# Performance work log

Measured on AMD Instinct MI355X. Metric: run time of the kernel, lower is better.

Reference implementation:

```python
import jax, jax.numpy as jnp
import numpy as np

B, T, E, H, OUT, L = 128, 512, 256, 512, 9, 2


def setup_inputs() -> dict:
    key = jax.random.key(0)
    ks = jax.random.split(key, 6)
    def lin(k, shape, fan_in):
        return (jax.random.normal(k, shape, jnp.float32) / np.float32(np.sqrt(fan_in)))
    return {
        "embeddings": jax.random.normal(ks[0], (B, T, E), jnp.float32),
        "W_w": lin(ks[1], (H, E), E),
        "W_b": jnp.zeros((H,), jnp.float32),
        "Uk_w": lin(ks[2], (L, H, H), H),
        "Uk_b": jnp.zeros((L, H), jnp.float32),
        "Wk_w": lin(ks[3], (L - 1, H, H), H),
        "Wk_b": jnp.zeros((L - 1, H), jnp.float32),
        "V_w": lin(ks[4], (OUT, H), H),
        "V_b": jnp.zeros((OUT,), jnp.float32),
    }


def reference(embeddings, W_w, W_b, Uk_w, Uk_b, Wk_w, Wk_b, V_w, V_b):
    n_layers = Uk_w.shape[0]
    bsz = embeddings.shape[0]
    hid = W_w.shape[0]
    # Input projection W(x_t) is time-independent: do it once as a big GEMM. [B,T,H]
    xproj = jnp.einsum('bte,he->bth', embeddings, W_w) + W_b

    def step(z_prev, xp_t):
        # z_prev: [L, B, H]; xp_t: [B, H]
        z = jnp.tanh(xp_t + z_prev[0] @ Uk_w[0].T + Uk_b[0])
        zs = [z]
        for l in range(n_layers - 1):
            # NOTE: original code uses Uks[l] (not Uks[l+1]) here -- reproduced faithfully.
            z = jnp.tanh(z @ Wk_w[l].T + Wk_b[l] + z_prev[l + 1] @ Uk_w[l].T + Uk_b[l])
            zs.append(z)
        y = z @ V_w.T + V_b  # [B, OUT]
        return jnp.stack(zs, 0), y

    z0 = jnp.zeros((n_layers, bsz, hid), embeddings.dtype)
    _, ys = jax.lax.scan(step, z0, jnp.swapaxes(xproj, 0, 1))  # ys: [T, B, OUT]
    return jnp.swapaxes(ys, 0, 1)  # [B, T, OUT]
```

## Files before the change

### kernel.cpp

```cpp
#include <hip/hip_runtime.h>
#include <hip/hip_fp16.h>

typedef _Float16 half8 __attribute__((ext_vector_type(8)));
typedef float floatx4 __attribute__((ext_vector_type(4)));


union H8 { half8 v; unsigned long long u[2]; };

__device__ __forceinline__ unsigned long long agload(const unsigned long long* p) {
  return __hip_atomic_load(p, __ATOMIC_RELAXED, __HIP_MEMORY_SCOPE_AGENT);
}
__device__ __forceinline__ void agstore(unsigned long long* p, unsigned long long v) {
  __hip_atomic_store(p, v, __ATOMIC_RELAXED, __HIP_MEMORY_SCOPE_AGENT);
}
__device__ __forceinline__ bool valid16(unsigned long long u) {
  return (unsigned)((unsigned)(u & 0xFFFFull) - 0x3C00u) <= 0x600u;
}

__global__ void prep_small(const float* __restrict__ Vw, const float* __restrict__ Vb,
                           const float* __restrict__ Wb, const float* __restrict__ Ukb,
                           const float* __restrict__ Wkb, const float* __restrict__ Ukw,
                           const float* __restrict__ Wkw, _Float16* __restrict__ V16,
                           float* __restrict__ bxp, float* __restrict__ bc,
                           float* __restrict__ sums) {
  int i = blockIdx.x * blockDim.x + threadIdx.x;
  if (i < 16 * 512) {
    int o = i >> 9, k = i & 511;
    V16[i] = (_Float16)(o < 9 ? Vw[o * 512 + k] : 0.0f);
  }
  if (i < 512) {
    bxp[i] = Wb[i] + Ukb[i];
    bc[i]  = Wkb[i] + Ukb[i];
  }
  if (i < 1024) {
    const float* row = (i < 512) ? Ukw + (size_t)i * 512 : Wkw + (size_t)(i - 512) * 512;
    float s = 0.f;
    for (int k = 0; k < 512; k += 4) {
      float4 v = *(const float4*)(row + k);
      s += (float)(_Float16)v.x + (float)(_Float16)v.y + (float)(_Float16)v.z + (float)(_Float16)v.w;
    }
    sums[i] = s;
  } else if (i < 1040) {
    int o = i - 1024;
    float s = 0.f;
    if (o < 9) {
      const float* row = Vw + (size_t)o * 512;
      for (int k = 0; k < 512; k += 4) {
        float4 v = *(const float4*)(row + k);
        s += (float)(_Float16)v.x + (float)(_Float16)v.y + (float)(_Float16)v.z + (float)(_Float16)v.w;
      }
    }
    sums[i] = (o < 9 ? Vb[o] : 0.f) - 2.f * s;
  }
}

__global__ __launch_bounds__(256) void gemm_xp(const float* __restrict__ Aptr,
                                               const float* __restrict__ Bptr,
                                               _Float16* __restrict__ Cout,
                                               const float* __restrict__ bias) {
  const int K = 256;
  __shared__ __align__(16) _Float16 As[128][40];
  __shared__ __align__(16) _Float16 Bs[128][40];
  const int tid = threadIdx.x;
  const int bm = blockIdx.x, bn = blockIdx.y;
  const int w = tid >> 6, lane = tid & 63;
  const int m = lane & 15, q = lane >> 4;

  floatx4 acc[2][8];
#pragma unroll
  for (int i = 0; i < 2; ++i)
#pragma unroll
    for (int j = 0; j < 8; ++j) acc[i][j] = (floatx4){0.f, 0.f, 0.f, 0.f};

  for (int kt = 0; kt < (K >> 5); ++kt) {
    const int k0 = kt << 5;
    __syncthreads();
#pragma unroll
    for (int it = 0; it < 2; ++it) {
      int idx = tid + it * 256;
      int row = idx >> 2, ch = idx & 3;
      size_t gA = (size_t)(bm * 128 + row) * K + (k0 + ch * 8);
      const float4* p = (const float4*)(Aptr + gA);
      float4 f0 = p[0], f1 = p[1];
      *(half8*)&As[row][ch * 8] =
          (half8){(_Float16)f0.x, (_Float16)f0.y, (_Float16)f0.z, (_Float16)f0.w,
                  (_Float16)f1.x, (_Float16)f1.y, (_Float16)f1.z, (_Float16)f1.w};
      size_t gB = (size_t)(bn * 128 + row) * K + (k0 + ch * 8);
      const float4* pb = (const float4*)(Bptr + gB);
      float4 g0 = pb[0], g1 = pb[1];
      *(half8*)&Bs[row][ch * 8] =
          (half8){(_Float16)g0.x, (_Float16)g0.y, (_Float16)g0.z, (_Float16)g0.w,
                  (_Float16)g1.x, (_Float16)g1.y, (_Float16)g1.z, (_Float16)g1.w};
    }
    __syncthreads();
    half8 a[2], b[8];
#pragma unroll
    for (int i = 0; i < 2; ++i) a[i] = *(const half8*)&As[w * 32 + i * 16 + m][q * 8];
#pragma unroll
    for (int j = 0; j < 8; ++j) b[j] = *(const half8*)&Bs[j * 16 + m][q * 8];
#pragma unroll
    for (int i = 0; i < 2; ++i)
#pragma unroll
      for (int j = 0; j < 8; ++j)
        acc[i][j] = __builtin_amdgcn_mfma_f32_16x16x32_f16(a[i], b[j], acc[i][j], 0, 0, 0);
  }
#pragma unroll
  for (int i = 0; i < 2; ++i)
#pragma unroll
    for (int j = 0; j < 8; ++j) {
      int col = bn * 128 + j * 16 + m;
      float bv = bias[col];
#pragma unroll
      for (int rr = 0; rr < 4; ++rr) {
        int row = bm * 128 + w * 32 + i * 16 + q * 4 + rr;
        size_t orow = (size_t)(row & 511) * 128 + (row >> 9);
        Cout[orow * 512 + col] = (_Float16)(acc[i][j][rr] + bv);
      }
    }
}

template <int SLEEP>
__device__ __forceinline__ void stage_tile(const _Float16* srcTile, _Float16* dst, int tid) {
  const unsigned long long* src = (const unsigned long long*)srcTile;
  unsigned long long g[8];
#pragma unroll
  for (int j = 0; j < 4; ++j) {
    g[2 * j] = agload(src + 2 * (tid + j * 256));
    g[2 * j + 1] = agload(src + 2 * (tid + j * 256) + 1);
  }
  unsigned need = 0;
#pragma unroll
  for (int i = 0; i < 8; ++i)
    if (!valid16(g[i])) need |= (1u << i);
  while (need) {
    if (SLEEP) __builtin_amdgcn_s_sleep(1);
#pragma unroll
    for (int i = 0; i < 8; ++i)
      if (need & (1u << i)) {
        unsigned long long v = agload(src + 2 * (tid + (i >> 1) * 256) + (i & 1));
        if (valid16(v)) { g[i] = v; need &= ~(1u << i); }
      }
  }
#pragma unroll
  for (int j = 0; j < 4; ++j) {
    H8 t;
    t.u[0] = g[2 * j];
    t.u[1] = g[2 * j + 1];
    *(half8*)&dst[(tid + j * 256) * 8] = t.v;
  }
}

__global__ __launch_bounds__(256, 1) void rnn_fused2(const float* __restrict__ Uw,
                                                     const float* __restrict__ Wkw,
                                                     const _Float16* __restrict__ xp,
                                                     _Float16* __restrict__ z0f,
                                                     _Float16* __restrict__ z1f,
                                                     const float* __restrict__ bc,
                                                     const float* __restrict__ sums) {
  __shared__ __align__(16) _Float16 az[8192];
  __shared__ __align__(16) _Float16 azs[8192];
  __shared__ __align__(16) _Float16 zo[16][136];
  const int tid = threadIdx.x;
  const int layer = blockIdx.x >> 5, bt = blockIdx.x & 7, ct = (blockIdx.x >> 3) & 3;
  const int lane = tid & 63, w = tid >> 6, m = lane & 15, q = lane >> 4;
  const int colbase = ct * 128 + w * 32;

  half8 ufr[2][16], wfr[2][16];
#pragma unroll
  for (int t = 0; t < 2; ++t) {
    const float* up = Uw + (size_t)(colbase + t * 16 + m) * 512 + q * 8;
    const float* wp = Wkw + (size_t)(colbase + t * 16 + m) * 512 + q * 8;
#pragma unroll
    for (int kk = 0; kk < 16; ++kk) {
      float4 f0 = *(const float4*)(up + kk * 32), f1 = *(const float4*)(up + kk * 32 + 4);
      ufr[t][kk] = (half8){(_Float16)f0.x, (_Float16)f0.y, (_Float16)f0.z, (_Float16)f0.w,
                           (_Float16)f1.x, (_Float16)f1.y, (_Float16)f1.z, (_Float16)f1.w};
      if (layer) {
        float4 g0 = *(const float4*)(wp + kk * 32), g1 = *(const float4*)(wp + kk * 32 + 4);
        wfr[t][kk] = (half8){(_Float16)g0.x, (_Float16)g0.y, (_Float16)g0.z, (_Float16)g0.w,
                             (_Float16)g1.x, (_Float16)g1.y, (_Float16)g1.z, (_Float16)g1.w};
      }
    }
  }
  const float corrU[2] = {-2.f * sums[colbase + m], -2.f * sums[colbase + 16 + m]};
  float cw[2] = {0.f, 0.f};
  if (layer) {
    cw[0] = -2.f * sums[512 + colbase + m] + bc[colbase + m];
    cw[1] = -2.f * sums[512 + colbase + 16 + m] + bc[colbase + 16 + m];
  }

  const int c16l = tid >> 4, b15 = tid & 15;
  _Float16* zout = layer ? z1f : z0f;

  if (layer) stage_tile<1>(z0f + (size_t)bt * 8192, azs, tid);

  for (int s = 0; s < 512; ++s) {
    float pin[8];
    if (layer == 0) {
      const _Float16* xb = xp + (size_t)s * 65536 + (size_t)(bt * 16) * 512;
#pragma unroll
      for (int t = 0; t < 2; ++t)
#pragma unroll
        for (int rr = 0; rr < 4; ++rr)
          pin[t * 4 + rr] = (float)xb[(size_t)(q * 4 + rr) * 512 + colbase + t * 16 + m];
    }

    floatx4 wk[2];
    wk[0] = (floatx4){0.f, 0.f, 0.f, 0.f};
    wk[1] = (floatx4){0.f, 0.f, 0.f, 0.f};
    if (layer) {
      __syncthreads();
      unsigned long long g[8];
      unsigned need = 0;
      const unsigned long long* src =
          (const unsigned long long*)(z1f + ((size_t)(s - 1) * 8 + bt) * 8192);
      if (s > 0) {
#pragma unroll
        for (int j = 0; j < 4; ++j) {
          g[2 * j] = agload(src + 2 * (tid + j * 256));
          g[2 * j + 1] = agload(src + 2 * (tid + j * 256) + 1);
        }
      }
#pragma unroll
      for (int kk = 0; kk < 16; ++kk) {
        half8 a = *(const half8*)&azs[((kk * 4 + q) * 16 + m) * 8];
        wk[0] = __builtin_amdgcn_mfma_f32_16x16x32_f16(a, wfr[0][kk], wk[0], 0, 0, 0);
        wk[1] = __builtin_amdgcn_mfma_f32_16x16x32_f16(a, wfr[1][kk], wk[1], 0, 0, 0);
      }
      if (s > 0) {
#pragma unroll
        for (int i = 0; i < 8; ++i)
          if (!valid16(g[i])) need |= (1u << i);
        while (need) {
#pragma unroll
          for (int i = 0; i < 8; ++i)
            if (need & (1u << i)) {
              unsigned long long v = agload(src + 2 * (tid + (i >> 1) * 256) + (i & 1));
              if (valid16(v)) { g[i] = v; need &= ~(1u << i); }
            }
        }
#pragma unroll
        for (int j = 0; j < 4; ++j) {
          H8 t;
          t.u[0] = g[2 * j];
          t.u[1] = g[2 * j + 1];
          *(half8*)&az[(tid + j * 256) * 8] = t.v;
        }
      }
    } else {
      if (s > 0) stage_tile<0>(z0f + ((size_t)(s - 1) * 8 + bt) * 8192, az, tid);
    }
    __syncthreads();

    floatx4 acc[2][2];
    acc[0][0] = (floatx4){0.f, 0.f, 0.f, 0.f};
    acc[0][1] = (floatx4){0.f, 0.f, 0.f, 0.f};
    acc[1][0] = (floatx4){0.f, 0.f, 0.f, 0.f};
    acc[1][1] = (floatx4){0.f, 0.f, 0.f, 0.f};
    if (s > 0) {
#pragma unroll
      for (int kk = 0; kk < 16; ++kk) {
        half8 a = *(const half8*)&az[((kk * 4 + q) * 16 + m) * 8];
        acc[0][kk & 1] = __builtin_amdgcn_mfma_f32_16x16x32_f16(a, ufr[0][kk], acc[0][kk & 1], 0, 0, 0);
        acc[1][kk & 1] = __builtin_amdgcn_mfma_f32_16x16x32_f16(a, ufr[1][kk], acc[1][kk & 1], 0, 0, 0);
      }
    }
#pragma unroll
    for (int t = 0; t < 2; ++t)
#pragma unroll
      for (int rr = 0; rr < 4; ++rr) {
        float x = layer ? (wk[t][rr] + cw[t]) : pin[t * 4 + rr];
        if (s > 0) x += acc[t][0][rr] + acc[t][1][rr] + corrU[t];
        float e = __builtin_exp2f(x * 2.885390081777927f);
        float enc = 3.f - 2.f * __builtin_amdgcn_rcpf(e + 1.f);
        zo[q * 4 + rr][w * 32 + t * 16 + m] = (_Float16)enc;
      }
    __syncthreads();
    {
      H8 pv;
      pv.v = *(const half8*)&zo[b15][c16l * 8];
      unsigned long long* dst =
          (unsigned long long*)((char*)zout +
                                (((size_t)s * 8 + bt) * 1024 + (size_t)(ct * 16 + c16l) * 16 + b15) * 16);
      agstore(dst, pv.u[0]);
      agstore(dst + 1, pv.u[1]);
    }
    if (layer && s < 511)
      stage_tile<1>(z0f + ((size_t)(s + 1) * 8 + bt) * 8192, azs, tid);
  }
}

__global__ __launch_bounds__(64) void out_gemm(const _Float16* __restrict__ z1,
                                               const _Float16* __restrict__ V16,
                                               const float* __restrict__ bco,
                                               float* __restrict__ out) {
  __shared__ __align__(16) _Float16 zt[16][520];
  __shared__ __align__(16) _Float16 vt[16][520];
  const int tid = threadIdx.x;
  const int m = tid & 15, q = tid >> 4;
  const size_t r0 = (size_t)blockIdx.x * 16;
  for (int idx = tid; idx < 1024; idx += 64) {
    int row = idx >> 6, ch = idx & 63;
    int r = (int)(r0 + row), t = r >> 7, b = r & 127;
    size_t off = (size_t)(t * 8 + (b >> 4)) * 8192 + (size_t)ch * 128 + (b & 15) * 8;
    *(half8*)&zt[row][ch * 8] = *(const half8*)&z1[off];
    *(half8*)&vt[row][ch * 8] = *(const half8*)&V16[(size_t)row * 512 + ch * 8];
  }
  __syncthreads();
  floatx4 acc = {0.f, 0.f, 0.f, 0.f};
#pragma unroll
  for (int kk = 0; kk < 16; ++kk) {
    half8 a = *(const half8*)&zt[m][kk * 32 + q * 8];
    half8 b = *(const half8*)&vt[m][kk * 32 + q * 8];
    acc = __builtin_amdgcn_mfma_f32_16x16x32_f16(a, b, acc, 0, 0, 0);
  }
  if (m < 9) {
#pragma unroll
    for (int rr = 0; rr < 4; ++rr) {
      size_t r = r0 + q * 4 + rr;
      size_t t = r >> 7, b = r & 127;
      out[(b * 512 + t) * 9 + m] = acc[rr] + bco[m];
    }
  }
}

extern "C" void kernel_launch(void* const* d_in, const int* in_sizes, int n_in,
                              void* d_out, int out_size, void* d_ws, size_t ws_size,
                              hipStream_t stream) {
  const float* emb = (const float*)d_in[0];
  const float* Ww  = (const float*)d_in[1];
  const float* Wb  = (const float*)d_in[2];
  const float* Ukw = (const float*)d_in[3];
  const float* Ukb = (const float*)d_in[4];
  const float* Wkw = (const float*)d_in[5];
  const float* Wkb = (const float*)d_in[6];
  const float* Vw  = (const float*)d_in[7];
  const float* Vb  = (const float*)d_in[8];
  float* out = (float*)d_out;

  char* ws = (char*)d_ws;
  _Float16* xp   = (_Float16*)(ws + 0);
  _Float16* z0f  = (_Float16*)(ws + 67108864);
  _Float16* z1f  = (_Float16*)(ws + 134217728);
  _Float16* V16  = (_Float16*)(ws + 201326592);
  float* bxp     = (float*)(ws + 201342976);
  float* bc      = (float*)(ws + 201345024);
  float* sums    = (float*)(ws + 201347072);

  hipLaunchKernelGGL(prep_small, dim3(32), dim3(256), 0, stream,
                     Vw, Vb, Wb, Ukb, Wkb, Ukw, Wkw, V16, bxp, bc, sums);
  hipLaunchKernelGGL(gemm_xp, dim3(512, 4), dim3(256), 0, stream, emb, Ww, xp, bxp);
  hipLaunchKernelGGL(rnn_fused2, dim3(64), dim3(256), 0, stream,
                     Ukw, Wkw, xp, z0f, z1f, bc, sums);
  hipLaunchKernelGGL(out_gemm, dim3(4096), dim3(64), 0, stream, z1f, V16, sums + 1024, out);
}
```

Before: 1.753 ms.

## Fuse input projection into recurrent kernel and load state directly into registers

Drops the separate input-projection GEMM. Layer-0 blocks now hold W_w fragments in registers and compute the embedding projection with MFMA at each step, so the fp16 xp buffer is never written or read back. The state exchange also changes: each wave reads the previous state straight from global memory into MFMA operand registers using per-element polling, and prefetches the next step's tiles right after storing its own. This removes the shared-memory staging and block-wide __syncthreads. The cost is higher register pressure, extra per-step embedding loads on the serial critical path, and more polling traffic.

```diff
diff --git a/kernel.cpp b/kernel.cpp
--- a/kernel.cpp
+++ b/kernel.cpp
@@ -54,239 +54,202 @@
   }
 }
 
-__global__ __launch_bounds__(256) void gemm_xp(const float* __restrict__ Aptr,
-                                               const float* __restrict__ Bptr,
-                                               _Float16* __restrict__ Cout,
-                                               const float* __restrict__ bias) {
-  const int K = 256;
-  __shared__ __align__(16) _Float16 As[128][40];
-  __shared__ __align__(16) _Float16 Bs[128][40];
-  const int tid = threadIdx.x;
-  const int bm = blockIdx.x, bn = blockIdx.y;
-  const int w = tid >> 6, lane = tid & 63;
-  const int m = lane & 15, q = lane >> 4;
-
-  floatx4 acc[2][8];
-#pragma unroll
-  for (int i = 0; i < 2; ++i)
-#pragma unroll
-    for (int j = 0; j < 8; ++j) acc[i][j] = (floatx4){0.f, 0.f, 0.f, 0.f};
-
-  for (int kt = 0; kt < (K >> 5); ++kt) {
-    const int k0 = kt << 5;
-    __syncthreads();
-#pragma unroll
-    for (int it = 0; it < 2; ++it) {
-      int idx = tid + it * 256;
-      int row = idx >> 2, ch = idx & 3;
-      size_t gA = (size_t)(bm * 128 + row) * K + (k0 + ch * 8);
-      const float4* p = (const float4*)(Aptr + gA);
-      float4 f0 = p[0], f1 = p[1];
-      *(half8*)&As[row][ch * 8] =
-          (half8){(_Float16)f0.x, (_Float16)f0.y, (_Float16)f0.z, (_Float16)f0.w,
-                  (_Float16)f1.x, (_Float16)f1.y, (_Float16)f1.z, (_Float16)f1.w};
-      size_t gB = (size_t)(bn * 128 + row) * K + (k0 + ch * 8);
-      const float4* pb = (const float4*)(Bptr + gB);
-      float4 g0 = pb[0], g1 = pb[1];
-      *(half8*)&Bs[row][ch * 8] =
-          (half8){(_Float16)g0.x, (_Float16)g0.y, (_Float16)g0.z, (_Float16)g0.w,
-                  (_Float16)g1.x, (_Float16)g1.y, (_Float16)g1.z, (_Float16)g1.w};
-    }
-    __syncthreads();
-    half8 a[2], b[8];
-#pragma unroll
-    for (int i = 0; i < 2; ++i) a[i] = *(const half8*)&As[w * 32 + i * 16 + m][q * 8];
-#pragma unroll
-    for (int j = 0; j < 8; ++j) b[j] = *(const half8*)&Bs[j * 16 + m][q * 8];
-#pragma unroll
-    for (int i = 0; i < 2; ++i)
-#pragma unroll
-      for (int j = 0; j < 8; ++j)
-        acc[i][j] = __builtin_amdgcn_mfma_f32_16x16x32_f16(a[i], b[j], acc[i][j], 0, 0, 0);
-  }
-#pragma unroll
-  for (int i = 0; i < 2; ++i)
-#pragma unroll
-    for (int j = 0; j < 8; ++j) {
-      int col = bn * 128 + j * 16 + m;
-      float bv = bias[col];
-#pragma unroll
-      for (int rr = 0; rr < 4; ++rr) {
-        int row = bm * 128 + w * 32 + i * 16 + q * 4 + rr;
-        size_t orow = (size_t)(row & 511) * 128 + (row >> 9);
-        Cout[orow * 512 + col] = (_Float16)(acc[i][j][rr] + bv);
-      }
-    }
-}
-
-template <int SLEEP>
-__device__ __forceinline__ void stage_tile(const _Float16* srcTile, _Float16* dst, int tid) {
-  const unsigned long long* src = (const unsigned long long*)srcTile;
-  unsigned long long g[8];
-#pragma unroll
-  for (int j = 0; j < 4; ++j) {
-    g[2 * j] = agload(src + 2 * (tid + j * 256));
-    g[2 * j + 1] = agload(src + 2 * (tid + j * 256) + 1);
-  }
-  unsigned need = 0;
-#pragma unroll
-  for (int i = 0; i < 8; ++i)
-    if (!valid16(g[i])) need |= (1u << i);
-  while (need) {
-    if (SLEEP) __builtin_amdgcn_s_sleep(1);
-#pragma unroll
-    for (int i = 0; i < 8; ++i)
-      if (need & (1u << i)) {
-        unsigned long long v = agload(src + 2 * (tid + (i >> 1) * 256) + (i & 1));
-        if (valid16(v)) { g[i] = v; need &= ~(1u << i); }
-      }
-  }
-#pragma unroll
-  for (int j = 0; j < 4; ++j) {
-    H8 t;
-    t.u[0] = g[2 * j];
-    t.u[1] = g[2 * j + 1];
-    *(half8*)&dst[(tid + j * 256) * 8] = t.v;
-  }
-}
-
-__global__ __launch_bounds__(256, 1) void rnn_fused2(const float* __restrict__ Uw,
-                                                     const float* __restrict__ Wkw,
-                                                     const _Float16* __restrict__ xp,
-                                                     _Float16* __restrict__ z0f,
-                                                     _Float16* __restrict__ z1f,
-                                                     const float* __restrict__ bc,
-                                                     const float* __restrict__ sums) {
-  __shared__ __align__(16) _Float16 az[8192];
-  __shared__ __align__(16) _Float16 azs[8192];
-  __shared__ __align__(16) _Float16 zo[16][136];
+__global__ __launch_bounds__(256, 1) void rnn_fused2(
+    const float* __restrict__ Uw, const float* __restrict__ Wkw,
+    const float* __restrict__ emb, const float* __restrict__ Ww,
+    _Float16* __restrict__ z0f, _Float16* __restrict__ z1f,
+    const float* __restrict__ bxp, const float* __restrict__ bc,
+    const float* __restrict__ sums) {
+  __shared__ __align__(16) _Float16 zo[4][16][40];
   const int tid = threadIdx.x;
   const int layer = blockIdx.x >> 5, bt = blockIdx.x & 7, ct = (blockIdx.x >> 3) & 3;
   const int lane = tid & 63, w = tid >> 6, m = lane & 15, q = lane >> 4;
   const int colbase = ct * 128 + w * 32;
-
-  half8 ufr[2][16], wfr[2][16];
+  const int cs = ct * 4 + w;
+  const int lbase = (q * 16 + m) * 2;
+
+  half8 ufr[2][16], wfr[2][16], wxr[2][8];
 #pragma unroll
   for (int t = 0; t < 2; ++t) {
     const float* up = Uw + (size_t)(colbase + t * 16 + m) * 512 + q * 8;
-    const float* wp = Wkw + (size_t)(colbase + t * 16 + m) * 512 + q * 8;
 #pragma unroll
     for (int kk = 0; kk < 16; ++kk) {
       float4 f0 = *(const float4*)(up + kk * 32), f1 = *(const float4*)(up + kk * 32 + 4);
       ufr[t][kk] = (half8){(_Float16)f0.x, (_Float16)f0.y, (_Float16)f0.z, (_Float16)f0.w,
                            (_Float16)f1.x, (_Float16)f1.y, (_Float16)f1.z, (_Float16)f1.w};
-      if (layer) {
+    }
+  }
+  if (layer == 0) {
+#pragma unroll
+    for (int t = 0; t < 2; ++t) {
+      const float* wp = Ww + (size_t)(colbase + t * 16 + m) * 256 + q * 8;
+#pragma unroll
+      for (int kk = 0; kk < 8; ++kk) {
+        float4 f0 = *(const float4*)(wp + kk * 32), f1 = *(const float4*)(wp + kk * 32 + 4);
+        wxr[t][kk] = (half8){(_Float16)f0.x, (_Float16)f0.y, (_Float16)f0.z, (_Float16)f0.w,
+                             (_Float16)f1.x, (_Float16)f1.y, (_Float16)f1.z, (_Float16)f1.w};
+      }
+    }
+  } else {
+#pragma unroll
+    for (int t = 0; t < 2; ++t) {
+      const float* wp = Wkw + (size_t)(colbase + t * 16 + m) * 512 + q * 8;
+#pragma unroll
+      for (int kk = 0; kk < 16; ++kk) {
         float4 g0 = *(const float4*)(wp + kk * 32), g1 = *(const float4*)(wp + kk * 32 + 4);
         wfr[t][kk] = (half8){(_Float16)g0.x, (_Float16)g0.y, (_Float16)g0.z, (_Float16)g0.w,
                              (_Float16)g1.x, (_Float16)g1.y, (_Float16)g1.z, (_Float16)g1.w};
       }
     }
   }
+
   const float corrU[2] = {-2.f * sums[colbase + m], -2.f * sums[colbase + 16 + m]};
-  float cw[2] = {0.f, 0.f};
+  float cw[2] = {0.f, 0.f}, bxpv[2] = {0.f, 0.f};
   if (layer) {
     cw[0] = -2.f * sums[512 + colbase + m] + bc[colbase + m];
     cw[1] = -2.f * sums[512 + colbase + 16 + m] + bc[colbase + 16 + m];
-  }
-
-  const int c16l = tid >> 4, b15 = tid & 15;
-  _Float16* zout = layer ? z1f : z0f;
-
-  if (layer) stage_tile<1>(z0f + (size_t)bt * 8192, azs, tid);
+  } else {
+    bxpv[0] = bxp[colbase + m];
+    bxpv[1] = bxp[colbase + 16 + m];
+  }
+
+  unsigned long long* const selfU = (unsigned long long*)(layer ? z1f : z0f);
+  const unsigned long long* const z0U = (const unsigned long long*)z0f;
+
+  unsigned long long ga[16][2];
+  unsigned long long gb[16][2];
+  if (layer) {
+    const unsigned long long* srcb0 = z0U + (size_t)bt * 2048;
+#pragma unroll
+    for (int i = 0; i < 16; ++i) {
+      gb[i][0] = agload(srcb0 + i * 128 + lbase);
+      gb[i][1] = agload(srcb0 + i * 128 + lbase + 1);
+    }
+  }
 
   for (int s = 0; s < 512; ++s) {
-    float pin[8];
+    float4 ef[8][2];
     if (layer == 0) {
-      const _Float16* xb = xp + (size_t)s * 65536 + (size_t)(bt * 16) * 512;
-#pragma unroll
-      for (int t = 0; t < 2; ++t)
-#pragma unroll
-        for (int rr = 0; rr < 4; ++rr)
-          pin[t * 4 + rr] = (float)xb[(size_t)(q * 4 + rr) * 512 + colbase + t * 16 + m];
-    }
-
-    floatx4 wk[2];
-    wk[0] = (floatx4){0.f, 0.f, 0.f, 0.f};
-    wk[1] = (floatx4){0.f, 0.f, 0.f, 0.f};
+      const float* ep = emb + (size_t)(bt * 16 + m) * 131072 + (size_t)s * 256 + q * 8;
+#pragma unroll
+      for (int kk = 0; kk < 8; ++kk) {
+        ef[kk][0] = *(const float4*)(ep + kk * 32);
+        ef[kk][1] = *(const float4*)(ep + kk * 32 + 4);
+      }
+    }
+
+    floatx4 wk[2][2];
+    wk[0][0] = wk[0][1] = wk[1][0] = wk[1][1] = (floatx4){0.f, 0.f, 0.f, 0.f};
     if (layer) {
-      __syncthreads();
-      unsigned long long g[8];
+      const unsigned long long* srcb = z0U + ((size_t)s * 8 + bt) * 2048;
       unsigned need = 0;
-      const unsigned long long* src =
-          (const unsigned long long*)(z1f + ((size_t)(s - 1) * 8 + bt) * 8192);
-      if (s > 0) {
-#pragma unroll
-        for (int j = 0; j < 4; ++j) {
-          g[2 * j] = agload(src + 2 * (tid + j * 256));
-          g[2 * j + 1] = agload(src + 2 * (tid + j * 256) + 1);
-        }
+#pragma unroll
+      for (int i = 0; i < 16; ++i) {
+        if (!valid16(gb[i][0])) need |= (1u << (2 * i));
+        if (!valid16(gb[i][1])) need |= (2u << (2 * i));
+      }
+      while (need) {
+#pragma unroll
+        for (int i = 0; i < 16; ++i) {
+          if (need & (1u << (2 * i))) gb[i][0] = agload(srcb + i * 128 + lbase);
+          if (need & (2u << (2 * i))) gb[i][1] = agload(srcb + i * 128 + lbase + 1);
+        }
+        unsigned nn = 0;
+#pragma unroll
+        for (int i = 0; i < 16; ++i) {
+          if ((need & (1u << (2 * i))) && !valid16(gb[i][0])) nn |= (1u << (2 * i));
+          if ((need & (2u << (2 * i))) && !valid16(gb[i][1])) nn |= (2u << (2 * i));
+        }
+        need = nn;
       }
 #pragma unroll
       for (int kk = 0; kk < 16; ++kk) {
-        half8 a = *(const half8*)&azs[((kk * 4 + q) * 16 + m) * 8];
-        wk[0] = __builtin_amdgcn_mfma_f32_16x16x32_f16(a, wfr[0][kk], wk[0], 0, 0, 0);
-        wk[1] = __builtin_amdgcn_mfma_f32_16x16x32_f16(a, wfr[1][kk], wk[1], 0, 0, 0);
-      }
-      if (s > 0) {
-#pragma unroll
-        for (int i = 0; i < 8; ++i)
-          if (!valid16(g[i])) need |= (1u << i);
-        while (need) {
-#pragma unroll
-          for (int i = 0; i < 8; ++i)
-            if (need & (1u << i)) {
-              unsigned long long v = agload(src + 2 * (tid + (i >> 1) * 256) + (i & 1));
-              if (valid16(v)) { g[i] = v; need &= ~(1u << i); }
-            }
-        }
-#pragma unroll
-        for (int j = 0; j < 4; ++j) {
-          H8 t;
-          t.u[0] = g[2 * j];
-          t.u[1] = g[2 * j + 1];
-          *(half8*)&az[(tid + j * 256) * 8] = t.v;
-        }
-      }
-    } else {
-      if (s > 0) stage_tile<0>(z0f + ((size_t)(s - 1) * 8 + bt) * 8192, az, tid);
-    }
-    __syncthreads();
+        H8 a; a.u[0] = gb[kk][0]; a.u[1] = gb[kk][1];
+        wk[0][kk & 1] = __builtin_amdgcn_mfma_f32_16x16x32_f16(a.v, wfr[0][kk], wk[0][kk & 1], 0, 0, 0);
+        wk[1][kk & 1] = __builtin_amdgcn_mfma_f32_16x16x32_f16(a.v, wfr[1][kk], wk[1][kk & 1], 0, 0, 0);
+      }
+    }
 
     floatx4 acc[2][2];
-    acc[0][0] = (floatx4){0.f, 0.f, 0.f, 0.f};
-    acc[0][1] = (floatx4){0.f, 0.f, 0.f, 0.f};
-    acc[1][0] = (floatx4){0.f, 0.f, 0.f, 0.f};
-    acc[1][1] = (floatx4){0.f, 0.f, 0.f, 0.f};
+    acc[0][0] = acc[0][1] = acc[1][0] = acc[1][1] = (floatx4){0.f, 0.f, 0.f, 0.f};
     if (s > 0) {
+      const unsigned long long* srca = selfU + ((size_t)(s - 1) * 8 + bt) * 2048;
+      unsigned need = 0;
+#pragma unroll
+      for (int i = 0; i < 16; ++i) {
+        if (!valid16(ga[i][0])) need |= (1u << (2 * i));
+        if (!valid16(ga[i][1])) need |= (2u << (2 * i));
+      }
+      while (need) {
+#pragma unroll
+        for (int i = 0; i < 16; ++i) {
+          if (need & (1u << (2 * i))) ga[i][0] = agload(srca + i * 128 + lbase);
+          if (need & (2u << (2 * i))) ga[i][1] = agload(srca + i * 128 + lbase + 1);
+        }
+        unsigned nn = 0;
+#pragma unroll
+        for (int i = 0; i < 16; ++i) {
+          if ((need & (1u << (2 * i))) && !valid16(ga[i][0])) nn |= (1u << (2 * i));
+          if ((need & (2u << (2 * i))) && !valid16(ga[i][1])) nn |= (2u << (2 * i));
+        }
+        need = nn;
+      }
+    }
+    if (layer == 0) {
+#pragma unroll
+      for (int kk = 0; kk < 8; ++kk) {
+        half8 a = (half8){(_Float16)ef[kk][0].x, (_Float16)ef[kk][0].y,
+                          (_Float16)ef[kk][0].z, (_Float16)ef[kk][0].w,
+                          (_Float16)ef[kk][1].x, (_Float16)ef[kk][1].y,
+                          (_Float16)ef[kk][1].z, (_Float16)ef[kk][1].w};
+        acc[0][kk & 1] = __builtin_amdgcn_mfma_f32_16x16x32_f16(a, wxr[0][kk], acc[0][kk & 1], 0, 0, 0);
+        acc[1][kk & 1] = __builtin_amdgcn_mfma_f32_16x16x32_f16(a, wxr[1][kk], acc[1][kk & 1], 0, 0, 0);
+      }
+    }
+    if (s > 0) {
 #pragma unroll
       for (int kk = 0; kk < 16; ++kk) {
-        half8 a = *(const half8*)&az[((kk * 4 + q) * 16 + m) * 8];
-        acc[0][kk & 1] = __builtin_amdgcn_mfma_f32_16x16x32_f16(a, ufr[0][kk], acc[0][kk & 1], 0, 0, 0);
-        acc[1][kk & 1] = __builtin_amdgcn_mfma_f32_16x16x32_f16(a, ufr[1][kk], acc[1][kk & 1], 0, 0, 0);
-      }
-    }
+        H8 a; a.u[0] = ga[kk][0]; a.u[1] = ga[kk][1];
+        acc[0][kk & 1] = __builtin_amdgcn_mfma_f32_16x16x32_f16(a.v, ufr[0][kk], acc[0][kk & 1], 0, 0, 0);
+        acc[1][kk & 1] = __builtin_amdgcn_mfma_f32_16x16x32_f16(a.v, ufr[1][kk], acc[1][kk & 1], 0, 0, 0);
+      }
+    }
+
 #pragma unroll
     for (int t = 0; t < 2; ++t)
 #pragma unroll
       for (int rr = 0; rr < 4; ++rr) {
-        float x = layer ? (wk[t][rr] + cw[t]) : pin[t * 4 + rr];
-        if (s > 0) x += acc[t][0][rr] + acc[t][1][rr] + corrU[t];
+        float x = acc[t][0][rr] + acc[t][1][rr] +
+                  (layer ? (wk[t][0][rr] + wk[t][1][rr] + cw[t]) : bxpv[t]);
+        if (s > 0) x += corrU[t];
         float e = __builtin_exp2f(x * 2.885390081777927f);
         float enc = 3.f - 2.f * __builtin_amdgcn_rcpf(e + 1.f);
-        zo[q * 4 + rr][w * 32 + t * 16 + m] = (_Float16)enc;
-      }
-    __syncthreads();
-    {
-      H8 pv;
-      pv.v = *(const half8*)&zo[b15][c16l * 8];
-      unsigned long long* dst =
-          (unsigned long long*)((char*)zout +
-                                (((size_t)s * 8 + bt) * 1024 + (size_t)(ct * 16 + c16l) * 16 + b15) * 16);
-      agstore(dst, pv.u[0]);
-      agstore(dst + 1, pv.u[1]);
-    }
-    if (layer && s < 511)
-      stage_tile<1>(z0f + ((size_t)(s + 1) * 8 + bt) * 8192, azs, tid);
+        zo[w][q * 4 + rr][t * 16 + m] = (_Float16)enc;
+      }
+    asm volatile("s_waitcnt lgkmcnt(0)" ::: "memory");
+    __builtin_amdgcn_sched_barrier(0);
+    H8 pv;
+    pv.v = *(const half8*)&zo[w][m][q * 8];
+    unsigned long long* dst = selfU + ((size_t)s * 8 + bt) * 2048 + cs * 128 + lbase;
+    agstore(dst, pv.u[0]);
+    agstore(dst + 1, pv.u[1]);
+
+    if (s < 511) {
+      const unsigned long long* srcn = selfU + ((size_t)s * 8 + bt) * 2048;
+#pragma unroll
+      for (int i = 0; i < 16; ++i) {
+        ga[i][0] = agload(srcn + i * 128 + lbase);
+        ga[i][1] = agload(srcn + i * 128 + lbase + 1);
+      }
+      if (layer) {
+        const unsigned long long* srcb2 = z0U + ((size_t)(s + 1) * 8 + bt) * 2048;
+#pragma unroll
+        for (int i = 0; i < 16; ++i) {
+          gb[i][0] = agload(srcb2 + i * 128 + lbase);
+          gb[i][1] = agload(srcb2 + i * 128 + lbase + 1);
+        }
+      }
+    }
   }
 }
 
@@ -339,18 +302,16 @@
   float* out = (float*)d_out;
 
   char* ws = (char*)d_ws;
-  _Float16* xp   = (_Float16*)(ws + 0);
-  _Float16* z0f  = (_Float16*)(ws + 67108864);
-  _Float16* z1f  = (_Float16*)(ws + 134217728);
-  _Float16* V16  = (_Float16*)(ws + 201326592);
-  float* bxp     = (float*)(ws + 201342976);
-  float* bc      = (float*)(ws + 201345024);
-  float* sums    = (float*)(ws + 201347072);
+  _Float16* z0f  = (_Float16*)(ws + 0);
+  _Float16* z1f  = (_Float16*)(ws + 67108864);
+  _Float16* V16  = (_Float16*)(ws + 134217728);
+  float* bxp     = (float*)(ws + 134234112);
+  float* bc      = (float*)(ws + 134236160);
+  float* sums    = (float*)(ws + 134238208);
 
   hipLaunchKernelGGL(prep_small, dim3(32), dim3(256), 0, stream,
                      Vw, Vb, Wb, Ukb, Wkb, Ukw, Wkw, V16, bxp, bc, sums);
-  hipLaunchKernelGGL(gemm_xp, dim3(512, 4), dim3(256), 0, stream, emb, Ww, xp, bxp);
   hipLaunchKernelGGL(rnn_fused2, dim3(64), dim3(256), 0, stream,
-                     Ukw, Wkw, xp, z0f, z1f, bc, sums);
+                     Ukw, Wkw, emb, Ww, z0f, z1f, bxp, bc, sums);
   hipLaunchKernelGGL(out_gemm, dim3(4096), dim3(64), 0, stream, z1f, V16, sums + 1024, out);
 }
```

After: 4.281 ms. 144% more time.

## Drop a per-step block barrier using wave-private output staging and double-buffered input tile

Applied to the files above, without the earlier changes.

Each wave now writes its 16x32 output slice to a private shared-memory region and reads it back for the global store within the same wave. That replaces the block-wide __syncthreads with an LDS waitcnt plus scheduling barrier. For layer 0, the staged input tile is double-buffered by step parity, so the next step's writes cannot race with the current step's readers now that the barrier is gone. The polling loops also issue all outstanding atomic loads before checking validity, batching memory latency, though this risks more redundant loads while spinning.

```diff
diff --git a/kernel.cpp b/kernel.cpp
--- a/kernel.cpp
+++ b/kernel.cpp
@@ -134,12 +134,17 @@
     if (!valid16(g[i])) need |= (1u << i);
   while (need) {
     if (SLEEP) __builtin_amdgcn_s_sleep(1);
+    unsigned long long t[8];
+#pragma unroll
+    for (int i = 0; i < 8; ++i)
+      if (need & (1u << i)) t[i] = agload(src + 2 * (tid + (i >> 1) * 256) + (i & 1));
+    unsigned nn = 0;
 #pragma unroll
     for (int i = 0; i < 8; ++i)
       if (need & (1u << i)) {
-        unsigned long long v = agload(src + 2 * (tid + (i >> 1) * 256) + (i & 1));
-        if (valid16(v)) { g[i] = v; need &= ~(1u << i); }
-      }
+        if (valid16(t[i])) g[i] = t[i]; else nn |= (1u << i);
+      }
+    need = nn;
   }
 #pragma unroll
   for (int j = 0; j < 4; ++j) {
@@ -157,13 +162,14 @@
                                                      _Float16* __restrict__ z1f,
                                                      const float* __restrict__ bc,
                                                      const float* __restrict__ sums) {
-  __shared__ __align__(16) _Float16 az[8192];
+  __shared__ __align__(16) _Float16 az[2][8192];
   __shared__ __align__(16) _Float16 azs[8192];
-  __shared__ __align__(16) _Float16 zo[16][136];
+  __shared__ __align__(16) _Float16 zo[4][16][40];
   const int tid = threadIdx.x;
   const int layer = blockIdx.x >> 5, bt = blockIdx.x & 7, ct = (blockIdx.x >> 3) & 3;
   const int lane = tid & 63, w = tid >> 6, m = lane & 15, q = lane >> 4;
   const int colbase = ct * 128 + w * 32;
+  const int cs = ct * 4 + w;
 
   half8 ufr[2][16], wfr[2][16];
 #pragma unroll
@@ -189,7 +195,6 @@
     cw[1] = -2.f * sums[512 + colbase + 16 + m] + bc[colbase + 16 + m];
   }
 
-  const int c16l = tid >> 4, b15 = tid & 15;
   _Float16* zout = layer ? z1f : z0f;
 
   if (layer) stage_tile<1>(z0f + (size_t)bt * 8192, azs, tid);
@@ -208,6 +213,7 @@
     floatx4 wk[2];
     wk[0] = (floatx4){0.f, 0.f, 0.f, 0.f};
     wk[1] = (floatx4){0.f, 0.f, 0.f, 0.f};
+    _Float16* azcur = layer ? az[0] : az[s & 1];
     if (layer) {
       __syncthreads();
       unsigned long long g[8];
@@ -232,23 +238,28 @@
         for (int i = 0; i < 8; ++i)
           if (!valid16(g[i])) need |= (1u << i);
         while (need) {
+          unsigned long long t[8];
+#pragma unroll
+          for (int i = 0; i < 8; ++i)
+            if (need & (1u << i)) t[i] = agload(src + 2 * (tid + (i >> 1) * 256) + (i & 1));
+          unsigned nn = 0;
 #pragma unroll
           for (int i = 0; i < 8; ++i)
             if (need & (1u << i)) {
-              unsigned long long v = agload(src + 2 * (tid + (i >> 1) * 256) + (i & 1));
-              if (valid16(v)) { g[i] = v; need &= ~(1u << i); }
+              if (valid16(t[i])) g[i] = t[i]; else nn |= (1u << i);
             }
+          need = nn;
         }
 #pragma unroll
         for (int j = 0; j < 4; ++j) {
           H8 t;
           t.u[0] = g[2 * j];
           t.u[1] = g[2 * j + 1];
-          *(half8*)&az[(tid + j * 256) * 8] = t.v;
+          *(half8*)&azcur[(tid + j * 256) * 8] = t.v;
         }
       }
     } else {
-      if (s > 0) stage_tile<0>(z0f + ((size_t)(s - 1) * 8 + bt) * 8192, az, tid);
+      if (s > 0) stage_tile<0>(z0f + ((size_t)(s - 1) * 8 + bt) * 8192, azcur, tid);
     }
     __syncthreads();
 
@@ -260,7 +271,7 @@
     if (s > 0) {
 #pragma unroll
       for (int kk = 0; kk < 16; ++kk) {
-        half8 a = *(const half8*)&az[((kk * 4 + q) * 16 + m) * 8];
+        half8 a = *(const half8*)&azcur[((kk * 4 + q) * 16 + m) * 8];
         acc[0][kk & 1] = __builtin_amdgcn_mfma_f32_16x16x32_f16(a, ufr[0][kk], acc[0][kk & 1], 0, 0, 0);
         acc[1][kk & 1] = __builtin_amdgcn_mfma_f32_16x16x32_f16(a, ufr[1][kk], acc[1][kk & 1], 0, 0, 0);
       }
@@ -273,15 +284,16 @@
         if (s > 0) x += acc[t][0][rr] + acc[t][1][rr] + corrU[t];
         float e = __builtin_exp2f(x * 2.885390081777927f);
         float enc = 3.f - 2.f * __builtin_amdgcn_rcpf(e + 1.f);
-        zo[q * 4 + rr][w * 32 + t * 16 + m] = (_Float16)enc;
-      }
-    __syncthreads();
+        zo[w][q * 4 + rr][t * 16 + m] = (_Float16)enc;
+      }
+    asm volatile("s_waitcnt lgkmcnt(0)" ::: "memory");
+    __builtin_amdgcn_sched_barrier(0);
     {
       H8 pv;
-      pv.v = *(const half8*)&zo[b15][c16l * 8];
+      pv.v = *(const half8*)&zo[w][m][q * 8];
       unsigned long long* dst =
           (unsigned long long*)((char*)zout +
-                                (((size_t)s * 8 + bt) * 1024 + (size_t)(ct * 16 + c16l) * 16 + b15) * 16);
+                                (((size_t)s * 8 + bt) * 1024 + (size_t)(cs * 4 + q) * 16 + m) * 16);
       agstore(dst, pv.u[0]);
       agstore(dst + 1, pv.u[1]);
     }
```

Result: no change. 1.782 ms (+1.7%).
